# Kernel tuning notes

Measured on AMD Instinct MI355X. Metric: run time of the kernel, lower is better.

Reference implementation:

```python
import jax, jax.numpy as jnp
import numpy as np

B, S, E, H = 4, 2048, 1024, 16
Dh = E // H
EPS = 1e-5


def setup_inputs() -> dict:
    key = jax.random.key(0)
    ks = jax.random.split(key, 16)
    w = lambda k, shp: jax.random.normal(k, shp, dtype=jnp.float32) * 0.02
    return {
        "x": jax.random.normal(ks[0], (B, S, E), dtype=jnp.float32),
        "Wq": w(ks[1], (E, E)), "bq": jnp.zeros((E,), jnp.float32),
        "Wk": w(ks[2], (E, E)), "bk": jnp.zeros((E,), jnp.float32),
        "Wv": w(ks[3], (E, E)), "bv": jnp.zeros((E,), jnp.float32),
        "Wo": w(ks[4], (E, E)), "bo": jnp.zeros((E,), jnp.float32),
        "an1_a": jnp.ones((1, S, 1), jnp.float32),
        "an1_b": jnp.zeros((1, S, 1), jnp.float32),
        "W1": w(ks[5], (2 * E, E)), "b1": jnp.zeros((2 * E,), jnp.float32),
        "W2": w(ks[6], (E, 2 * E)), "b2": jnp.zeros((E,), jnp.float32),
        "an2_a": jnp.ones((1, S, 1), jnp.float32),
        "an2_b": jnp.zeros((1, S, 1), jnp.float32),
    }


def adaptive_norm(x, a, b):
    # AdaptiveNorm((1, N_s, 1)): normalize over embedding dim, per-position affine.
    mu = jnp.mean(x, axis=-1, keepdims=True)
    var = jnp.mean(jnp.square(x - mu), axis=-1, keepdims=True)
    return a * (x - mu) * jax.lax.rsqrt(var + EPS) + b


def reference(x, Wq, bq, Wk, bk, Wv, bv, Wo, bo, an1_a, an1_b, W1, b1, W2, b2, an2_a, an2_b):
    scale = 1.0 / np.sqrt(E / H)
    # QKV projections -> (B, S, H, Dh)
    q = (x @ Wq.T + bq).reshape(B, S, H, Dh)
    k = (x @ Wk.T + bk).reshape(B, S, H, Dh)
    v = (x @ Wv.T + bv).reshape(B, S, H, Dh)
    # scaled dot-product attention (materializes B,H,S,S like the original)
    scores = jnp.einsum("bshd,bthd->bhst", q, k) * scale
    probs = jax.nn.softmax(scores, axis=-1)
    attn = jnp.einsum("bhst,bthd->bshd", probs, v).reshape(B, S, E)
    attn = attn @ Wo.T + bo
    # residual + adaptive norm (dropout is identity in eval mode)
    h = adaptive_norm(attn + x, an1_a, an1_b)
    ff = jax.nn.relu(h @ W1.T + b1) @ W2.T + b2
    out = adaptive_norm(ff + h, an2_a, an2_b)
    return out
```

## Files before the change

### kernel.cpp

```cpp
#include <hip/hip_runtime.h>


typedef __attribute__((ext_vector_type(8))) short s16x8;
typedef __attribute__((ext_vector_type(4))) short s16x4;
typedef __attribute__((ext_vector_type(4))) unsigned short u16x4;
typedef __attribute__((ext_vector_type(4))) float f32x4;

__device__ __forceinline__ float bf2f(unsigned short u) {
  unsigned int v = ((unsigned int)u) << 16;
  return __builtin_bit_cast(float, v);
}
__device__ __forceinline__ unsigned short f2bf(float f) {
  unsigned int u = __builtin_bit_cast(unsigned int, f);
  u += 0x7fffu + ((u >> 16) & 1u);
  return (unsigned short)(u >> 16);
}
__device__ __forceinline__ unsigned int pkbf_trunc(float f0, float f1) {
  return __builtin_amdgcn_perm(__builtin_bit_cast(unsigned int, f1),
                               __builtin_bit_cast(unsigned int, f0), 0x07060302u);
}
__device__ __forceinline__ f32x4 mfma16(s16x8 a, s16x8 b, f32x4 c) {
  return __builtin_amdgcn_mfma_f32_16x16x32_bf16(a, b, c, 0, 0, 0);
}
__device__ __forceinline__ void gl2lds16(const unsigned short* g, unsigned short* l) {
  __builtin_amdgcn_global_load_lds(
      (const __attribute__((address_space(1))) unsigned int*)(g),
      (__attribute__((address_space(3))) unsigned int*)(l), 16, 0, 0);
}

__global__ void detect_dtype(const unsigned int* __restrict__ x, int* __restrict__ flag) {
  const int tid = threadIdx.x;
  int cnt = 0;
  for (int i = tid; i < 2048; i += 256) {
    const unsigned e = (x[i] >> 7) & 0xFF;
    cnt += (e >= 100 && e <= 150) ? 1 : 0;
  }
#pragma unroll
  for (int off = 32; off >= 1; off >>= 1) cnt += __shfl_xor(cnt, off);
  __shared__ int red[4];
  if ((tid & 63) == 0) red[tid >> 6] = cnt;
  __syncthreads();
  if (tid == 0) *flag = ((red[0] + red[1] + red[2] + red[3]) > 1536) ? 1 : 0;
}

struct CvtArgs {
  const void* src[17];
  unsigned short* dst[17];
  int cum4[18];
};

__global__ __launch_bounds__(256) void cvt_all(CvtArgs a, const int* __restrict__ flag, int total4) {
  const int i = blockIdx.x * 256 + threadIdx.x;
  if (i >= total4) return;
  int lo = 0, hi = 17;
  while (hi - lo > 1) {
    const int mid = (lo + hi) >> 1;
    if (i >= a.cum4[mid]) lo = mid; else hi = mid;
  }
  const int off4 = i - a.cum4[lo];
  if (*flag) {
    const u16x4* s = (const u16x4*)a.src[lo];
    *(u16x4*)&a.dst[lo][off4 * 4] = s[off4];
  } else {
    const float4* s = (const float4*)a.src[lo];
    const float4 v = s[off4];
    u16x4 o;
    o[0] = f2bf(v.x); o[1] = f2bf(v.y); o[2] = f2bf(v.z); o[3] = f2bf(v.w);
    *(u16x4*)&a.dst[lo][off4 * 4] = o;
  }
}

#define BM 128
#define BN 128
#define BKK 64
#define QOFF 8388608L
#define SCALE2 0.18033688011f

template <int EPI>
__global__ __launch_bounds__(256, 2) void gemm_bt(
    const unsigned short* __restrict__ A, const unsigned short* __restrict__ W,
    const unsigned short* __restrict__ bias, const unsigned short* __restrict__ resid,
    unsigned short* __restrict__ out, int M, int N, int K) {
  __shared__ unsigned short Al[BM * BKK];
  __shared__ unsigned short Bl[BN * BKK];
  const int tid = threadIdx.x;
  const int lane = tid & 63;
  const int wave = tid >> 6;
  const int qd = lane >> 4;
  const int c = lane & 15;
  const int wm = (wave >> 1) * 64;
  const int wn = (wave & 1) * 64;
  const long m0 = (long)blockIdx.y * BM;
  const long n0 = (long)blockIdx.x * BN;

  f32x4 acc[4][4] = {};

  const int scc = ((tid & 7) ^ ((tid >> 3) & 7)) * 8;
  const unsigned short* Ag = A + (m0 + (tid >> 3)) * (long)K + scc;
  const unsigned short* Wg = W + (n0 + (tid >> 3)) * (long)K + scc;

  for (int k0 = 0; k0 < K; k0 += BKK) {
    __syncthreads();
#pragma unroll
    for (int p = 0; p < 4; ++p)
      gl2lds16(Ag + (long)p * 32 * K + k0, &Al[(p * 256 + tid) * 8]);
#pragma unroll
    for (int p = 0; p < 4; ++p)
      gl2lds16(Wg + (long)p * 32 * K + k0, &Bl[(p * 256 + tid) * 8]);
    __syncthreads();
#pragma unroll
    for (int ks = 0; ks < 2; ++ks) {
      const int ch = ((ks * 4 + qd) ^ (c & 7)) * 8;
      s16x8 af[4], bfr[4];
#pragma unroll
      for (int mt = 0; mt < 4; ++mt)
        af[mt] = *(const s16x8*)&Al[(wm + mt * 16 + c) * BKK + ch];
#pragma unroll
      for (int nt = 0; nt < 4; ++nt)
        bfr[nt] = *(const s16x8*)&Bl[(wn + nt * 16 + c) * BKK + ch];
#pragma unroll
      for (int mt = 0; mt < 4; ++mt)
#pragma unroll
        for (int nt = 0; nt < 4; ++nt)
          acc[mt][nt] = mfma16(af[mt], bfr[nt], acc[mt][nt]);
    }
  }

#pragma unroll
  for (int nt = 0; nt < 4; ++nt) {
    const int gn = (int)n0 + wn + nt * 16 + c;
    const float bv = bf2f(bias[gn]);
#pragma unroll
    for (int mt = 0; mt < 4; ++mt) {
      const long gmb = m0 + wm + mt * 16 + qd * 4;
      if constexpr (EPI == 2) {
#pragma unroll
        for (int r = 0; r < 4; ++r) {
          const long gm = gmb + r;
          const float v = acc[mt][nt][r] + bv + bf2f(resid[gm * N + gn]);
          out[gm * N + gn] = f2bf(v);
        }
      } else if constexpr (EPI == 3) {
#pragma unroll
        for (int r = 0; r < 4; ++r) {
          const long gm = gmb + r;
          float v = acc[mt][nt][r] + bv;
          v = fmaxf(v, 0.0f);
          out[gm * N + gn] = f2bf(v);
        }
      } else {
        const int seg = gn >> 10;
        const int nn = gn & 1023;
        const int h = nn >> 6, d = nn & 63;
        if (seg == 0) {
#pragma unroll
          for (int r = 0; r < 4; ++r) {
            const long gm = gmb + r;
            const long b = gm >> 11;
            const int s = (int)(gm & 2047);
            out[((b * 16 + h) * 2048L + s) * 64 + d] =
                f2bf((acc[mt][nt][r] + bv) * SCALE2);
          }
        } else if (seg == 1) {
#pragma unroll
          for (int r = 0; r < 4; ++r) {
            const long gm = gmb + r;
            const long b = gm >> 11;
            const int s = (int)(gm & 2047);
            (out + QOFF)[((b * 16 + h) * 2048L + s) * 64 + d] =
                f2bf(acc[mt][nt][r] + bv);
          }
        } else {
          const long b = gmb >> 11;
          const int s = (int)(gmb & 2047);
          s16x4 pv;
#pragma unroll
          for (int r = 0; r < 4; ++r) pv[r] = (short)f2bf(acc[mt][nt][r] + bv);
          *(s16x4*)&(out + 2 * QOFF)[((b * 16 + h) * 64L + d) * 2048 + s] = pv;
        }
      }
    }
  }
}

#define ATT_S 2048

__global__ __launch_bounds__(256)
__attribute__((amdgpu_waves_per_eu(2, 2))) void attn_fwd(
    const unsigned short* __restrict__ Q, const unsigned short* __restrict__ K,
    const unsigned short* __restrict__ VT, unsigned short* __restrict__ O) {
  __shared__ unsigned short SH[32768];
  unsigned short* Kl = SH;
  unsigned short* VTl = SH + 128 * 64;
  unsigned short* Pl = SH + 128 * 64 + 64 * 128;

  const int bh = blockIdx.y;
  const int q0 = blockIdx.x * 256;
  const unsigned short* Qh = Q + (long)bh * ATT_S * 64;
  const unsigned short* Kg = K + (long)bh * ATT_S * 64;
  const unsigned short* Vg = VT + (long)bh * 64 * ATT_S;

  const int tid = threadIdx.x;
  const int wave = tid >> 6, lane = tid & 63;
  const int qd = lane >> 4, c = lane & 15;
  const int mb = wave * 32;

  s16x8 qf[2][2][2];
#pragma unroll
  for (int h2 = 0; h2 < 2; ++h2)
#pragma unroll
    for (int mt = 0; mt < 2; ++mt)
#pragma unroll
      for (int ks = 0; ks < 2; ++ks)
        qf[h2][mt][ks] = *(const s16x8*)&Qh[(long)(q0 + h2 * 128 + mb + mt * 16 + c) * 64 +
                                            ks * 32 + qd * 8];

  s16x8 ones;
#pragma unroll
  for (int i = 0; i < 8; ++i) ones[i] = (short)0x3F80;

  f32x4 oacc[2][4][2] = {};
  f32x4 lacc[2][2] = {};

  const int kscc = ((tid & 7) ^ ((tid >> 3) & 7)) * 8;
  const int vscc = ((tid & 15) ^ ((tid >> 4) & 15)) * 8;

  for (int kv = 0; kv < ATT_S; kv += 128) {
    __syncthreads();
#pragma unroll
    for (int p = 0; p < 4; ++p) {
      const int idx = p * 256 + tid;
      gl2lds16(Kg + (long)kv * 64 + (long)(idx >> 3) * 64 + kscc, &Kl[idx * 8]);
    }
#pragma unroll
    for (int p = 0; p < 4; ++p) {
      const int idx = p * 256 + tid;
      gl2lds16(Vg + (long)(idx >> 4) * ATT_S + kv + vscc,
               &VTl[(idx >> 4) * 128 + (idx & 15) * 8]);
    }
    __syncthreads();

#pragma unroll
    for (int h2 = 0; h2 < 2; ++h2) {
      f32x4 sacc[8][2] = {};
#pragma unroll
      for (int ks = 0; ks < 2; ++ks) {
        const int ch = ((ks * 4 + qd) ^ (c & 7)) * 8;
        s16x8 kf[8];
#pragma unroll
        for (int tt = 0; tt < 8; ++tt)
          kf[tt] = *(const s16x8*)&Kl[(tt * 16 + c) * 64 + ch];
#pragma unroll
        for (int mt = 0; mt < 2; ++mt)
#pragma unroll
          for (int tt = 0; tt < 8; ++tt)
            sacc[tt][mt] = mfma16(kf[tt], qf[h2][mt][ks], sacc[tt][mt]);
      }

#pragma unroll
      for (int mt = 0; mt < 2; ++mt) {
        const int ml = mb + mt * 16 + c;
#pragma unroll
        for (int tt = 0; tt < 8; ++tt) {
          unsigned int pk[2];
          pk[0] = pkbf_trunc(__builtin_amdgcn_exp2f(sacc[tt][mt][0]),
                             __builtin_amdgcn_exp2f(sacc[tt][mt][1]));
          pk[1] = pkbf_trunc(__builtin_amdgcn_exp2f(sacc[tt][mt][2]),
                             __builtin_amdgcn_exp2f(sacc[tt][mt][3]));
          const int chw = ((tt * 2 + (qd >> 1)) ^ (ml & 7)) * 8 + (qd & 1) * 4;
          *(uint2*)&Pl[ml * 128 + chw] = *(uint2*)pk;
        }
      }
      asm volatile("s_waitcnt lgkmcnt(0)" ::: "memory");

#pragma unroll
      for (int ks = 0; ks < 4; ++ks) {
        const int vch = ((ks * 4 + qd) ^ c) * 8;
        s16x8 vf[4], pf[2];
#pragma unroll
        for (int dt = 0; dt < 4; ++dt)
          vf[dt] = *(const s16x8*)&VTl[(dt * 16 + c) * 128 + vch];
#pragma unroll
        for (int mt = 0; mt < 2; ++mt) {
          const int pr = mb + mt * 16 + c;
          pf[mt] = *(const s16x8*)&Pl[pr * 128 + (((ks * 4 + qd) ^ (pr & 7)) * 8)];
        }
#pragma unroll
        for (int mt = 0; mt < 2; ++mt) {
#pragma unroll
          for (int dt = 0; dt < 4; ++dt)
            oacc[h2][dt][mt] = mfma16(vf[dt], pf[mt], oacc[h2][dt][mt]);
          lacc[h2][mt] = mfma16(ones, pf[mt], lacc[h2][mt]);
        }
      }
    }
  }

  const long b = bh >> 4;
  const int h = bh & 15;
#pragma unroll
  for (int h2 = 0; h2 < 2; ++h2)
#pragma unroll
    for (int mt = 0; mt < 2; ++mt) {
      const float inv = 1.0f / lacc[h2][mt][0];
      const int s = q0 + h2 * 128 + mb + mt * 16 + c;
      const long ob = (b * (long)ATT_S + s) * 1024L + h * 64;
#pragma unroll
      for (int dt = 0; dt < 4; ++dt) {
        s16x4 ov;
#pragma unroll
        for (int r = 0; r < 4; ++r) ov[r] = (short)f2bf(oacc[h2][dt][mt][r] * inv);
        *(s16x4*)&O[ob + dt * 16 + qd * 4] = ov;
      }
    }
}

template <bool FINAL>
__global__ __launch_bounds__(256) void norm_affine(
    const unsigned short* __restrict__ X, const unsigned short* __restrict__ av,
    const unsigned short* __restrict__ bv, void* __restrict__ outv,
    const int* __restrict__ flag) {
  const int row = blockIdx.x;
  const int s = row & 2047;
  const unsigned short* xr = X + (long)row * 1024;
  const int tid = threadIdx.x;
  const u16x4 u = *(const u16x4*)&xr[tid * 4];
  float v[4];
  float s1 = 0.f, s2 = 0.f;
#pragma unroll
  for (int i = 0; i < 4; ++i) {
    v[i] = bf2f(u[i]);
    s1 += v[i];
    s2 += v[i] * v[i];
  }
#pragma unroll
  for (int off = 32; off >= 1; off >>= 1) {
    s1 += __shfl_xor(s1, off);
    s2 += __shfl_xor(s2, off);
  }
  __shared__ float red[8];
  const int wave = tid >> 6, lane = tid & 63;
  if (lane == 0) {
    red[wave * 2] = s1;
    red[wave * 2 + 1] = s2;
  }
  __syncthreads();
  s1 = red[0] + red[2] + red[4] + red[6];
  s2 = red[1] + red[3] + red[5] + red[7];
  const float mean = s1 * (1.0f / 1024.0f);
  const float var = fmaxf(s2 * (1.0f / 1024.0f) - mean * mean, 0.0f);
  const float rstd = rsqrtf(var + 1e-5f);
  const float aa = bf2f(av[s]), bb = bf2f(bv[s]);
  float o[4];
#pragma unroll
  for (int i = 0; i < 4; ++i) o[i] = aa * (v[i] - mean) * rstd + bb;
  bool as_bf16 = true;
  if constexpr (FINAL) as_bf16 = (*flag != 0);
  if (as_bf16) {
    u16x4 ob;
#pragma unroll
    for (int i = 0; i < 4; ++i) ob[i] = f2bf(o[i]);
    *(u16x4*)&((unsigned short*)outv)[(long)row * 1024 + tid * 4] = ob;
  } else {
    float4 of = {o[0], o[1], o[2], o[3]};
    *(float4*)&((float*)outv)[(long)row * 1024 + tid * 4] = of;
  }
}

extern "C" void kernel_launch(void* const* d_in, const int* in_sizes, int n_in,
                              void* d_out, int out_size, void* d_ws, size_t ws_size,
                              hipStream_t stream) {
  char* ws = (char*)d_ws;
  const size_t SZ = 8192ull * 1024 * 2;
  const size_t WSZ = 1024ull * 1024 * 2;

  unsigned short* xb   = (unsigned short*)(ws);
  unsigned short* qb   = (unsigned short*)(ws + SZ);
  unsigned short* kb   = (unsigned short*)(ws + 2 * SZ);
  unsigned short* vtb  = (unsigned short*)(ws + 3 * SZ);
  unsigned short* attn = (unsigned short*)(ws + 4 * SZ);
  unsigned short* hb   = (unsigned short*)(ws + 5 * SZ);
  unsigned short* r1   = qb;
  unsigned short* ffb  = kb;
  unsigned short* r2   = attn;

  char* wreg = ws + 6 * SZ;
  unsigned short* wqb = (unsigned short*)(wreg);
  unsigned short* w1b = (unsigned short*)(wreg + 4 * WSZ);
  unsigned short* w2b = (unsigned short*)(wreg + 6 * WSZ);
  unsigned short* wob = (unsigned short*)(wreg + 3 * WSZ);
  unsigned short* smal = (unsigned short*)(wreg + 8 * WSZ);
  unsigned short* bqb = smal;
  unsigned short* bkb = smal + 1024;
  unsigned short* bvb = smal + 2048;
  unsigned short* bob = smal + 3072;
  unsigned short* b1b = smal + 4096;
  unsigned short* b2b = smal + 6144;
  unsigned short* a1b = smal + 7168;
  unsigned short* g1b = smal + 9216;
  unsigned short* a2b = smal + 11264;
  unsigned short* g2b = smal + 13312;
  int* flag = (int*)(wreg + 8 * WSZ + 64 * 1024);

  CvtArgs ca;
  unsigned short* wkb = wqb + 1024 * 1024;
  unsigned short* wvb = wqb + 2 * 1024 * 1024;
  unsigned short* dsts[17] = {xb, wqb, bqb, wkb, bkb, wvb, bvb, wob, bob,
                              a1b, g1b, w1b, b1b, w2b, b2b, a2b, g2b};
  ca.cum4[0] = 0;
  for (int i = 0; i < 17; ++i) {
    ca.src[i] = d_in[i];
    ca.dst[i] = dsts[i];
    ca.cum4[i + 1] = ca.cum4[i] + in_sizes[i] / 4;
  }
  const int total4 = ca.cum4[17];

  dim3 blk(256);
  detect_dtype<<<1, blk, 0, stream>>>((const unsigned int*)d_in[0], flag);
  cvt_all<<<(total4 + 255) / 256, blk, 0, stream>>>(ca, flag, total4);

  gemm_bt<4><<<dim3(24, 64), blk, 0, stream>>>(xb, wqb, bqb, nullptr, qb, 8192, 3072, 1024);
  attn_fwd<<<dim3(8, 64), blk, 0, stream>>>(qb, kb, vtb, attn);
  gemm_bt<2><<<dim3(8, 64), blk, 0, stream>>>(attn, wob, bob, xb, r1, 8192, 1024, 1024);
  norm_affine<false><<<8192, blk, 0, stream>>>(r1, a1b, g1b, hb, nullptr);
  gemm_bt<3><<<dim3(16, 64), blk, 0, stream>>>(hb, w1b, b1b, nullptr, ffb, 8192, 2048, 1024);
  gemm_bt<2><<<dim3(8, 64), blk, 0, stream>>>(ffb, w2b, b2b, hb, r2, 8192, 1024, 2048);
  norm_affine<true><<<8192, blk, 0, stream>>>(r2, a2b, g2b, d_out, flag);
}
```

Baseline: 455.0 us.

## Double-buffer K/V tiles in attention and keep Q/K in row-major token layout

The attention kernel now uses double-buffered 64-key K and V tiles in LDS. The next tile is prefetched with async global-to-LDS loads while the current one is computed, and a vmcnt wait plus barrier replaces the two full syncthreads per iteration. The QKV projection epilogue writes Q and K in plain row-major (B,S,E) layout rather than a head-major permuted layout, and the attention kernel reads them with a stride of 1024. Smaller KV tiles cut LDS use and add iterations, and the strided Q/K reads may coalesce less well.

```diff
diff --git a/kernel.cpp b/kernel.cpp
--- a/kernel.cpp
+++ b/kernel.cpp
@@ -151,26 +151,16 @@
       } else {
         const int seg = gn >> 10;
         const int nn = gn & 1023;
-        const int h = nn >> 6, d = nn & 63;
         if (seg == 0) {
 #pragma unroll
-          for (int r = 0; r < 4; ++r) {
-            const long gm = gmb + r;
-            const long b = gm >> 11;
-            const int s = (int)(gm & 2047);
-            out[((b * 16 + h) * 2048L + s) * 64 + d] =
-                f2bf((acc[mt][nt][r] + bv) * SCALE2);
-          }
+          for (int r = 0; r < 4; ++r)
+            out[(gmb + r) * 1024 + nn] = f2bf((acc[mt][nt][r] + bv) * SCALE2);
         } else if (seg == 1) {
 #pragma unroll
-          for (int r = 0; r < 4; ++r) {
-            const long gm = gmb + r;
-            const long b = gm >> 11;
-            const int s = (int)(gm & 2047);
-            (out + QOFF)[((b * 16 + h) * 2048L + s) * 64 + d] =
-                f2bf(acc[mt][nt][r] + bv);
-          }
+          for (int r = 0; r < 4; ++r)
+            (out + QOFF)[(gmb + r) * 1024 + nn] = f2bf(acc[mt][nt][r] + bv);
         } else {
+          const int h = nn >> 6, d = nn & 63;
           const long b = gmb >> 11;
           const int s = (int)(gmb & 2047);
           s16x4 pv;
@@ -189,22 +179,29 @@
 __attribute__((amdgpu_waves_per_eu(2, 2))) void attn_fwd(
     const unsigned short* __restrict__ Q, const unsigned short* __restrict__ K,
     const unsigned short* __restrict__ VT, unsigned short* __restrict__ O) {
-  __shared__ unsigned short SH[32768];
-  unsigned short* Kl = SH;
-  unsigned short* VTl = SH + 128 * 64;
-  unsigned short* Pl = SH + 128 * 64 + 64 * 128;
+  __shared__ unsigned short SH[24576];
+  unsigned short* Kb0 = SH;
+  unsigned short* Kb1 = SH + 4096;
+  unsigned short* Vb0 = SH + 8192;
+  unsigned short* Vb1 = SH + 12288;
+  unsigned short* Pl  = SH + 16384;
 
   const int bh = blockIdx.y;
   const int q0 = blockIdx.x * 256;
-  const unsigned short* Qh = Q + (long)bh * ATT_S * 64;
-  const unsigned short* Kg = K + (long)bh * ATT_S * 64;
-  const unsigned short* Vg = VT + (long)bh * 64 * ATT_S;
+  const long b = bh >> 4;
+  const int h = bh & 15;
+  const unsigned short* Qg = Q + (b * 2048) * 1024 + h * 64;
+  const unsigned short* Kg = K + (b * 2048) * 1024 + h * 64;
+  const unsigned short* Vg = VT + (long)bh * 64 * 2048;
 
   const int tid = threadIdx.x;
   const int wave = tid >> 6, lane = tid & 63;
   const int qd = lane >> 4, c = lane & 15;
   const int mb = wave * 32;
 
+  const int srow = tid >> 3;
+  const int sccs = ((tid & 7) ^ (srow & 7)) * 8;
+
   s16x8 qf[2][2][2];
 #pragma unroll
   for (int h2 = 0; h2 < 2; ++h2)
@@ -212,7 +209,7 @@
     for (int mt = 0; mt < 2; ++mt)
 #pragma unroll
       for (int ks = 0; ks < 2; ++ks)
-        qf[h2][mt][ks] = *(const s16x8*)&Qh[(long)(q0 + h2 * 128 + mb + mt * 16 + c) * 64 +
+        qf[h2][mt][ks] = *(const s16x8*)&Qg[(long)(q0 + h2 * 128 + mb + mt * 16 + c) * 1024 +
                                             ks * 32 + qd * 8];
 
   s16x8 ones;
@@ -222,38 +219,39 @@
   f32x4 oacc[2][4][2] = {};
   f32x4 lacc[2][2] = {};
 
-  const int kscc = ((tid & 7) ^ ((tid >> 3) & 7)) * 8;
-  const int vscc = ((tid & 15) ^ ((tid >> 4) & 15)) * 8;
-
-  for (int kv = 0; kv < ATT_S; kv += 128) {
-    __syncthreads();
-#pragma unroll
-    for (int p = 0; p < 4; ++p) {
-      const int idx = p * 256 + tid;
-      gl2lds16(Kg + (long)kv * 64 + (long)(idx >> 3) * 64 + kscc, &Kl[idx * 8]);
-    }
-#pragma unroll
-    for (int p = 0; p < 4; ++p) {
-      const int idx = p * 256 + tid;
-      gl2lds16(Vg + (long)(idx >> 4) * ATT_S + kv + vscc,
-               &VTl[(idx >> 4) * 128 + (idx & 15) * 8]);
-    }
-    __syncthreads();
+  gl2lds16(Kg + (long)srow * 1024 + sccs, &Kb0[tid * 8]);
+  gl2lds16(Kg + (long)(srow + 32) * 1024 + sccs, &Kb0[(256 + tid) * 8]);
+  gl2lds16(Vg + (long)srow * 2048 + sccs, &Vb0[tid * 8]);
+  gl2lds16(Vg + (long)(srow + 32) * 2048 + sccs, &Vb0[(256 + tid) * 8]);
+
+  for (int it = 0; it < 32; ++it) {
+    const int p = it & 1;
+    unsigned short* Kc = p ? Kb1 : Kb0;
+    unsigned short* Vc = p ? Vb1 : Vb0;
+    unsigned short* Kn = p ? Kb0 : Kb1;
+    unsigned short* Vn = p ? Vb0 : Vb1;
+    const int kvn = (it < 31) ? (it + 1) * 64 : 31 * 64;
+    gl2lds16(Kg + (long)(kvn + srow) * 1024 + sccs, &Kn[tid * 8]);
+    gl2lds16(Kg + (long)(kvn + srow + 32) * 1024 + sccs, &Kn[(256 + tid) * 8]);
+    gl2lds16(Vg + (long)srow * 2048 + kvn + sccs, &Vn[tid * 8]);
+    gl2lds16(Vg + (long)(srow + 32) * 2048 + kvn + sccs, &Vn[(256 + tid) * 8]);
+
+    asm volatile("s_waitcnt vmcnt(4)\n\ts_barrier" ::: "memory");
 
 #pragma unroll
     for (int h2 = 0; h2 < 2; ++h2) {
-      f32x4 sacc[8][2] = {};
+      f32x4 sacc[4][2] = {};
 #pragma unroll
       for (int ks = 0; ks < 2; ++ks) {
         const int ch = ((ks * 4 + qd) ^ (c & 7)) * 8;
-        s16x8 kf[8];
-#pragma unroll
-        for (int tt = 0; tt < 8; ++tt)
-          kf[tt] = *(const s16x8*)&Kl[(tt * 16 + c) * 64 + ch];
+        s16x8 kf[4];
+#pragma unroll
+        for (int tt = 0; tt < 4; ++tt)
+          kf[tt] = *(const s16x8*)&Kc[(tt * 16 + c) * 64 + ch];
 #pragma unroll
         for (int mt = 0; mt < 2; ++mt)
 #pragma unroll
-          for (int tt = 0; tt < 8; ++tt)
+          for (int tt = 0; tt < 4; ++tt)
             sacc[tt][mt] = mfma16(kf[tt], qf[h2][mt][ks], sacc[tt][mt]);
       }
 
@@ -261,29 +259,29 @@
       for (int mt = 0; mt < 2; ++mt) {
         const int ml = mb + mt * 16 + c;
 #pragma unroll
-        for (int tt = 0; tt < 8; ++tt) {
+        for (int tt = 0; tt < 4; ++tt) {
           unsigned int pk[2];
           pk[0] = pkbf_trunc(__builtin_amdgcn_exp2f(sacc[tt][mt][0]),
                              __builtin_amdgcn_exp2f(sacc[tt][mt][1]));
           pk[1] = pkbf_trunc(__builtin_amdgcn_exp2f(sacc[tt][mt][2]),
                              __builtin_amdgcn_exp2f(sacc[tt][mt][3]));
           const int chw = ((tt * 2 + (qd >> 1)) ^ (ml & 7)) * 8 + (qd & 1) * 4;
-          *(uint2*)&Pl[ml * 128 + chw] = *(uint2*)pk;
+          *(uint2*)&Pl[ml * 64 + chw] = *(uint2*)pk;
         }
       }
       asm volatile("s_waitcnt lgkmcnt(0)" ::: "memory");
 
 #pragma unroll
-      for (int ks = 0; ks < 4; ++ks) {
-        const int vch = ((ks * 4 + qd) ^ c) * 8;
+      for (int ks = 0; ks < 2; ++ks) {
+        const int vch = ((ks * 4 + qd) ^ (c & 7)) * 8;
         s16x8 vf[4], pf[2];
 #pragma unroll
         for (int dt = 0; dt < 4; ++dt)
-          vf[dt] = *(const s16x8*)&VTl[(dt * 16 + c) * 128 + vch];
+          vf[dt] = *(const s16x8*)&Vc[(dt * 16 + c) * 64 + vch];
 #pragma unroll
         for (int mt = 0; mt < 2; ++mt) {
           const int pr = mb + mt * 16 + c;
-          pf[mt] = *(const s16x8*)&Pl[pr * 128 + (((ks * 4 + qd) ^ (pr & 7)) * 8)];
+          pf[mt] = *(const s16x8*)&Pl[pr * 64 + (((ks * 4 + qd) ^ (pr & 7)) * 8)];
         }
 #pragma unroll
         for (int mt = 0; mt < 2; ++mt) {
@@ -294,10 +292,10 @@
         }
       }
     }
-  }
-
-  const long b = bh >> 4;
-  const int h = bh & 15;
+
+    asm volatile("s_barrier" ::: "memory");
+  }
+
 #pragma unroll
   for (int h2 = 0; h2 < 2; ++h2)
 #pragma unroll
```

New measurement: 444.6 us. 1.02x faster.
